# Optimization experiments

Measured on AMD Instinct MI355X. Metric: run time of the kernel, lower is better.

The kernel has to match this reference:

```python
import jax, jax.numpy as jnp
import numpy as np

NODE_NUM = 100000
LAYER_NUM = 4
EMB = 128
FEAT = 256
BATCH = 4096
NEIGH = 32
EPS = 1e-12  # F.normalize default eps


def setup_inputs() -> dict:
    key = jax.random.key(0)
    ks = jax.random.split(key, 10)
    std = 1.0 / np.sqrt(EMB)
    return {
        "layers": jax.random.randint(ks[0], (BATCH,), 0, LAYER_NUM),
        "node_i": jax.random.randint(ks[1], (BATCH,), 0, NODE_NUM),
        "neighs_i": jax.random.randint(ks[2], (BATCH, LAYER_NUM, NEIGH), 0, NODE_NUM),
        "features": jax.random.normal(ks[3], (NODE_NUM, FEAT), dtype=jnp.float32),
        "layer_embs": jax.random.uniform(ks[4], (NODE_NUM, LAYER_NUM, EMB), dtype=jnp.float32, minval=-1.0, maxval=1.0),
        "neigh_emb_trans": jax.random.normal(ks[5], (LAYER_NUM, FEAT, EMB), dtype=jnp.float32) * std,
        "trans_weights": jax.random.normal(ks[6], (EMB, EMB), dtype=jnp.float32) * std,
        "trans_weights_s1": jax.random.normal(ks[7], (EMB, EMB), dtype=jnp.float32) * std,
        "trans_weights_s2": jax.random.normal(ks[8], (EMB, 1), dtype=jnp.float32) * std,
    }


def reference(layers, node_i, neighs_i, features, layer_embs, neigh_emb_trans,
              trans_weights, trans_weights_s1, trans_weights_s2):
    # Gather neighbor features: [B, L, J, F]
    feats_n = features[neighs_i]
    # Per-layer linear transform == diagonal of torch's 'bijk,akm->bijam' over (i,a):
    # [B, L, J, M]
    h = jnp.einsum('bljf,lfm->bljm', feats_n, neigh_emb_trans)
    # Sum over neighbors -> [B, L, M]
    h = h.sum(axis=2)
    # Attention over layers: tanh(h @ Ws1) @ Ws2 -> [B, L]
    scores = jnp.squeeze(jnp.tanh(h @ trans_weights_s1) @ trans_weights_s2, axis=-1)
    att = jax.nn.softmax(scores, axis=1)  # [B, L]
    # Attention-weighted layer aggregation -> [B, M]
    agg = jnp.einsum('bl,blm->bm', att, h)
    node_embed = agg @ trans_weights  # [B, M]
    final = node_embed + layer_embs[node_i, layers]  # residual with per-(node,layer) emb
    # F.normalize(dim=1): x / max(||x||_2, eps)
    norm = jnp.linalg.norm(final, axis=1, keepdims=True)
    return final / jnp.maximum(norm, EPS)
```

## Files before the change

### kernel.cpp

```cpp
#include <hip/hip_runtime.h>
#include <math.h>

#define BATCH 4096
#define LNUM  4
#define NEIGH 32
#define FEAT  256
#define EMB   128
#define NODES 100000

__device__ __forceinline__ unsigned int f2bf(float x) {
  unsigned int u = __float_as_uint(x);
  return (u + 0x7fffu + ((u >> 16) & 1u)) >> 16;
}

__global__ __launch_bounds__(256) void k_convert(
    const float* __restrict__ f, unsigned short* __restrict__ fb) {
  size_t i0 = ((size_t)blockIdx.x * 256 + threadIdx.x) * 8;
  float4 a = *(const float4*)(f + i0);
  float4 b = *(const float4*)(f + i0 + 4);
  uint4 o;
  o.x = f2bf(a.x) | (f2bf(a.y) << 16);
  o.y = f2bf(a.z) | (f2bf(a.w) << 16);
  o.z = f2bf(b.x) | (f2bf(b.y) << 16);
  o.w = f2bf(b.z) | (f2bf(b.w) << 16);
  *(uint4*)(fb + i0) = o;
}

__global__ __launch_bounds__(256, 2) void k12(
    const int* __restrict__ neighs, const unsigned short* __restrict__ fb,
    const float* __restrict__ W, float* __restrict__ H) {
  __shared__ float sS[32][260];
  __shared__ float sW[32][128];
  int b0 = blockIdx.x * 32;
  int l = blockIdx.y;
  int tid = threadIdx.x;
  int w = tid >> 6, lane = tid & 63;
  int half = lane >> 5;
  int seg = lane & 31;

  int idx[8];
#pragma unroll
  for (int i = 0; i < 8; ++i) {
    const int* nbr = neighs + ((size_t)(b0 + w * 8 + i) * LNUM + l) * NEIGH;
    idx[i] = nbr[seg];
  }
#pragma unroll
  for (int p = 0; p < 4; ++p) {
    float a[8] = {0.f, 0.f, 0.f, 0.f, 0.f, 0.f, 0.f, 0.f};
#pragma unroll
    for (int jj = 0; jj < 4; ++jj) {
      uint4 v[8];
#pragma unroll
      for (int q = 0; q < 8; ++q) {
        int j = jj * 8 + q;
        int nA = __shfl(idx[2 * p], j, 64);
        int nB = __shfl(idx[2 * p + 1], j, 64);
        int n = half ? nB : nA;
        v[q] = *((const uint4*)(fb + (size_t)n * FEAT) + seg);
      }
#pragma unroll
      for (int q = 0; q < 8; ++q) {
        a[0] += __uint_as_float(v[q].x << 16);
        a[1] += __uint_as_float(v[q].x & 0xffff0000u);
        a[2] += __uint_as_float(v[q].y << 16);
        a[3] += __uint_as_float(v[q].y & 0xffff0000u);
        a[4] += __uint_as_float(v[q].z << 16);
        a[5] += __uint_as_float(v[q].z & 0xffff0000u);
        a[6] += __uint_as_float(v[q].w << 16);
        a[7] += __uint_as_float(v[q].w & 0xffff0000u);
      }
    }
    int r = w * 8 + 2 * p + half;
    *(float4*)&sS[r][seg * 8] = make_float4(a[0], a[1], a[2], a[3]);
    *(float4*)&sS[r][seg * 8 + 4] = make_float4(a[4], a[5], a[6], a[7]);
  }
  __syncthreads();

  int tx = tid & 31;
  int ty = tid >> 5;
  float acc[4][4] = {};
  const float* Wl = W + (size_t)l * FEAT * EMB;
  for (int k0 = 0; k0 < FEAT; k0 += 32) {
#pragma unroll
    for (int t = 0; t < 4; ++t) {
      int i2 = tid + t * 256;
      int kk = i2 >> 5;
      int cc = i2 & 31;
      *(float4*)&sW[kk][cc * 4] =
          *(const float4*)&Wl[(size_t)(k0 + kk) * EMB + cc * 4];
    }
    __syncthreads();
#pragma unroll
    for (int kc = 0; kc < 32; kc += 4) {
      float4 s4[4];
#pragma unroll
      for (int r = 0; r < 4; ++r)
        s4[r] = *(const float4*)&sS[ty * 4 + r][k0 + kc];
#pragma unroll
      for (int kk = 0; kk < 4; ++kk) {
        float4 wv = *(const float4*)&sW[kc + kk][tx * 4];
#pragma unroll
        for (int r = 0; r < 4; ++r) {
          float sv = ((const float*)&s4[r])[kk];
          acc[r][0] += sv * wv.x; acc[r][1] += sv * wv.y;
          acc[r][2] += sv * wv.z; acc[r][3] += sv * wv.w;
        }
      }
    }
    __syncthreads();
  }
#pragma unroll
  for (int r = 0; r < 4; ++r) {
    int b = b0 + ty * 4 + r;
    *(float4*)&H[((size_t)b * LNUM + l) * EMB + tx * 4] =
        make_float4(acc[r][0], acc[r][1], acc[r][2], acc[r][3]);
  }
}

__global__ __launch_bounds__(256, 2) void k34(
    const float* __restrict__ H, const float* __restrict__ Ws1,
    const float* __restrict__ Ws2, const float* __restrict__ Wt,
    const int* __restrict__ node_i, const int* __restrict__ layers,
    const float* __restrict__ layer_embs, float* __restrict__ out) {
  __shared__ float sHH[64][130];
  __shared__ float sAgg[16][128];
  __shared__ float sc[64];
  int b0 = blockIdx.x * 16;
  int tid = threadIdx.x;
  int w = tid >> 6, lane = tid & 63;

  {
    const float4* Hp = (const float4*)(H + (size_t)b0 * LNUM * EMB);
    for (int i = tid; i < 64 * 32; i += 256) {
      int r = i >> 5, c = i & 31;
      *(float4*)&sHH[r][c * 4] = Hp[i];
    }
  }
  __syncthreads();

  {
    float acc[16][2] = {};
    for (int k = 0; k < EMB; k += 2) {
      float2 h2[16];
#pragma unroll
      for (int r = 0; r < 16; ++r)
        h2[r] = *(const float2*)&sHH[w * 16 + r][k];
      float2 w0 = *(const float2*)&Ws1[(size_t)k * EMB + lane * 2];
      float2 w1 = *(const float2*)&Ws1[(size_t)(k + 1) * EMB + lane * 2];
#pragma unroll
      for (int r = 0; r < 16; ++r) {
        acc[r][0] += h2[r].x * w0.x + h2[r].y * w1.x;
        acc[r][1] += h2[r].x * w0.y + h2[r].y * w1.y;
      }
    }
    float2 w2v = *(const float2*)&Ws2[lane * 2];
#pragma unroll
    for (int r = 0; r < 16; ++r) {
      float p = tanhf(acc[r][0]) * w2v.x + tanhf(acc[r][1]) * w2v.y;
#pragma unroll
      for (int m = 1; m < 64; m <<= 1) p += __shfl_xor(p, m, 64);
      if (lane == 0) sc[w * 16 + r] = p;
    }
  }
  __syncthreads();

  for (int i = tid; i < 16 * EMB; i += 256) {
    int lb = i >> 7, m = i & 127;
    float s0 = sc[lb * 4 + 0], s1 = sc[lb * 4 + 1];
    float s2 = sc[lb * 4 + 2], s3 = sc[lb * 4 + 3];
    float mx = fmaxf(fmaxf(s0, s1), fmaxf(s2, s3));
    float e0 = expf(s0 - mx), e1 = expf(s1 - mx);
    float e2 = expf(s2 - mx), e3 = expf(s3 - mx);
    float inv = 1.0f / (e0 + e1 + e2 + e3);
    float a = e0 * sHH[lb * 4 + 0][m] + e1 * sHH[lb * 4 + 1][m] +
              e2 * sHH[lb * 4 + 2][m] + e3 * sHH[lb * 4 + 3][m];
    sAgg[lb][m] = a * inv;
  }
  __syncthreads();

  {
    float ax[4] = {0.f, 0.f, 0.f, 0.f}, ay[4] = {0.f, 0.f, 0.f, 0.f};
    for (int k = 0; k < EMB; ++k) {
      float2 wv = *(const float2*)&Wt[(size_t)k * EMB + lane * 2];
#pragma unroll
      for (int g = 0; g < 4; ++g) {
        float a = sAgg[w * 4 + g][k];
        ax[g] += a * wv.x;
        ay[g] += a * wv.y;
      }
    }
#pragma unroll
    for (int g = 0; g < 4; ++g) {
      int b = b0 + w * 4 + g;
      int node = node_i[b];
      int lay = layers[b];
      float2 e = *(const float2*)&layer_embs[((size_t)node * LNUM + lay) * EMB +
                                             lane * 2];
      float vx = ax[g] + e.x, vy = ay[g] + e.y;
      float ss = vx * vx + vy * vy;
#pragma unroll
      for (int m = 1; m < 64; m <<= 1) ss += __shfl_xor(ss, m, 64);
      float inv = 1.0f / fmaxf(sqrtf(ss), 1e-12f);
      *(float2*)&out[(size_t)b * EMB + lane * 2] =
          make_float2(vx * inv, vy * inv);
    }
  }
}

extern "C" void kernel_launch(void* const* d_in, const int* in_sizes, int n_in,
                              void* d_out, int out_size, void* d_ws,
                              size_t ws_size, hipStream_t stream) {
  const int* layers = (const int*)d_in[0];
  const int* node_i = (const int*)d_in[1];
  const int* neighs = (const int*)d_in[2];
  const float* features = (const float*)d_in[3];
  const float* layer_embs = (const float*)d_in[4];
  const float* neigh_emb_trans = (const float*)d_in[5];
  const float* trans_weights = (const float*)d_in[6];
  const float* trans_weights_s1 = (const float*)d_in[7];
  const float* trans_weights_s2 = (const float*)d_in[8];
  float* out = (float*)d_out;

  unsigned short* fb = (unsigned short*)d_ws;
  float* H = (float*)((char*)d_ws + (size_t)NODES * FEAT * sizeof(unsigned short));

  k_convert<<<dim3(NODES * FEAT / (256 * 8)), 256, 0, stream>>>(features, fb);
  k12<<<dim3(BATCH / 32, LNUM), 256, 0, stream>>>(neighs, fb, neigh_emb_trans, H);
  k34<<<dim3(BATCH / 16), 256, 0, stream>>>(H, trans_weights_s1,
                                            trans_weights_s2, trans_weights,
                                            node_i, layers, layer_embs, out);
}
```

Baseline: 414.8 us.

## Drop bf16 conversion pass and gather fp32 features in node-range sweeps

Removes the kernel that converted the whole 100k x 256 feature table to bf16 before gathering. The gather kernel now reads fp32 features directly. It sweeps the node-id space in 32 slices, and each wave fetches only the neighbors whose index falls in the current slice, so concurrently running blocks touch the same region of the table and should get more L2/LLC hits. The cost is 32 ballot passes per row group, serialized per-neighbor loops, and twice the bytes per fetched row.

```diff
diff --git a/kernel.cpp b/kernel.cpp
--- a/kernel.cpp
+++ b/kernel.cpp
@@ -8,26 +8,11 @@
 #define EMB   128
 #define NODES 100000
 
-__device__ __forceinline__ unsigned int f2bf(float x) {
-  unsigned int u = __float_as_uint(x);
-  return (u + 0x7fffu + ((u >> 16) & 1u)) >> 16;
-}
-
-__global__ __launch_bounds__(256) void k_convert(
-    const float* __restrict__ f, unsigned short* __restrict__ fb) {
-  size_t i0 = ((size_t)blockIdx.x * 256 + threadIdx.x) * 8;
-  float4 a = *(const float4*)(f + i0);
-  float4 b = *(const float4*)(f + i0 + 4);
-  uint4 o;
-  o.x = f2bf(a.x) | (f2bf(a.y) << 16);
-  o.y = f2bf(a.z) | (f2bf(a.w) << 16);
-  o.z = f2bf(b.x) | (f2bf(b.y) << 16);
-  o.w = f2bf(b.z) | (f2bf(b.w) << 16);
-  *(uint4*)(fb + i0) = o;
-}
+#define NPASS 32
+#define SLICE (NODES / NPASS)
 
 __global__ __launch_bounds__(256, 2) void k12(
-    const int* __restrict__ neighs, const unsigned short* __restrict__ fb,
+    const int* __restrict__ neighs, const float* __restrict__ features,
     const float* __restrict__ W, float* __restrict__ H) {
   __shared__ float sS[32][260];
   __shared__ float sW[32][128];
@@ -35,50 +20,41 @@
   int l = blockIdx.y;
   int tid = threadIdx.x;
   int w = tid >> 6, lane = tid & 63;
-  int half = lane >> 5;
-  int seg = lane & 31;
 
   int idx[8];
 #pragma unroll
   for (int i = 0; i < 8; ++i) {
     const int* nbr = neighs + ((size_t)(b0 + w * 8 + i) * LNUM + l) * NEIGH;
-    idx[i] = nbr[seg];
-  }
-#pragma unroll
-  for (int p = 0; p < 4; ++p) {
-    float a[8] = {0.f, 0.f, 0.f, 0.f, 0.f, 0.f, 0.f, 0.f};
-#pragma unroll
-    for (int jj = 0; jj < 4; ++jj) {
-      uint4 v[8];
-#pragma unroll
-      for (int q = 0; q < 8; ++q) {
-        int j = jj * 8 + q;
-        int nA = __shfl(idx[2 * p], j, 64);
-        int nB = __shfl(idx[2 * p + 1], j, 64);
-        int n = half ? nB : nA;
-        v[q] = *((const uint4*)(fb + (size_t)n * FEAT) + seg);
-      }
-#pragma unroll
-      for (int q = 0; q < 8; ++q) {
-        a[0] += __uint_as_float(v[q].x << 16);
-        a[1] += __uint_as_float(v[q].x & 0xffff0000u);
-        a[2] += __uint_as_float(v[q].y << 16);
-        a[3] += __uint_as_float(v[q].y & 0xffff0000u);
-        a[4] += __uint_as_float(v[q].z << 16);
-        a[5] += __uint_as_float(v[q].z & 0xffff0000u);
-        a[6] += __uint_as_float(v[q].w << 16);
-        a[7] += __uint_as_float(v[q].w & 0xffff0000u);
-      }
-    }
-    int r = w * 8 + 2 * p + half;
-    *(float4*)&sS[r][seg * 8] = make_float4(a[0], a[1], a[2], a[3]);
-    *(float4*)&sS[r][seg * 8 + 4] = make_float4(a[4], a[5], a[6], a[7]);
-  }
+    idx[i] = nbr[lane & 31];
+  }
+  float4 acc[8];
+#pragma unroll
+  for (int i = 0; i < 8; ++i) acc[i] = make_float4(0.f, 0.f, 0.f, 0.f);
+
+  for (int p = 0; p < NPASS; ++p) {
+    int lo = p * SLICE;
+#pragma unroll
+    for (int i = 0; i < 8; ++i) {
+      bool inr = ((unsigned int)(idx[i] - lo)) < (unsigned int)SLICE;
+      unsigned long long m = __ballot(inr) & 0xffffffffull;
+      while (m) {
+        int j = __ffsll((long long)m) - 1;
+        m &= m - 1;
+        int n = __shfl(idx[i], j, 64);
+        float4 v = *((const float4*)(features + (size_t)n * FEAT) + lane);
+        acc[i].x += v.x; acc[i].y += v.y;
+        acc[i].z += v.z; acc[i].w += v.w;
+      }
+    }
+  }
+#pragma unroll
+  for (int i = 0; i < 8; ++i)
+    *(float4*)&sS[w * 8 + i][lane * 4] = acc[i];
   __syncthreads();
 
   int tx = tid & 31;
   int ty = tid >> 5;
-  float acc[4][4] = {};
+  float accO[4][4] = {};
   const float* Wl = W + (size_t)l * FEAT * EMB;
   for (int k0 = 0; k0 < FEAT; k0 += 32) {
 #pragma unroll
@@ -102,8 +78,8 @@
 #pragma unroll
         for (int r = 0; r < 4; ++r) {
           float sv = ((const float*)&s4[r])[kk];
-          acc[r][0] += sv * wv.x; acc[r][1] += sv * wv.y;
-          acc[r][2] += sv * wv.z; acc[r][3] += sv * wv.w;
+          accO[r][0] += sv * wv.x; accO[r][1] += sv * wv.y;
+          accO[r][2] += sv * wv.z; accO[r][3] += sv * wv.w;
         }
       }
     }
@@ -113,7 +89,7 @@
   for (int r = 0; r < 4; ++r) {
     int b = b0 + ty * 4 + r;
     *(float4*)&H[((size_t)b * LNUM + l) * EMB + tx * 4] =
-        make_float4(acc[r][0], acc[r][1], acc[r][2], acc[r][3]);
+        make_float4(accO[r][0], accO[r][1], accO[r][2], accO[r][3]);
   }
 }
 
@@ -221,11 +197,10 @@
   const float* trans_weights_s2 = (const float*)d_in[8];
   float* out = (float*)d_out;
 
-  unsigned short* fb = (unsigned short*)d_ws;
-  float* H = (float*)((char*)d_ws + (size_t)NODES * FEAT * sizeof(unsigned short));
-
-  k_convert<<<dim3(NODES * FEAT / (256 * 8)), 256, 0, stream>>>(features, fb);
-  k12<<<dim3(BATCH / 32, LNUM), 256, 0, stream>>>(neighs, fb, neigh_emb_trans, H);
+  float* H = (float*)d_ws;
+
+  k12<<<dim3(BATCH / 32, LNUM), 256, 0, stream>>>(neighs, features,
+                                                  neigh_emb_trans, H);
   k34<<<dim3(BATCH / 16), 256, 0, stream>>>(H, trans_weights_s1,
                                             trans_weights_s2, trans_weights,
                                             node_i, layers, layer_embs, out);
```

Result: slower. 463.6 us (+11.8%).
